# Kernel optimization log

Measured on AMD Instinct MI355X. Metric: run time of the kernel, lower is better.

The kernel has to match this reference:

```python
import jax, jax.numpy as jnp
import numpy as np


def setup_inputs() -> dict:
    key = jax.random.key(0)
    kx, ky = jax.random.split(key)
    x = jax.random.normal(kx, (16, 4096, 3), dtype=jnp.float32)
    y = jax.random.normal(ky, (16, 4096, 3), dtype=jnp.float32)
    return {"x": x, "y": y}


def reference(x, y):
    # avoiding the O(b*N*M*d) difference tensor of the naive expansion.
    x2 = jnp.sum(x * x, axis=-1)                  # (b, N)
    y2 = jnp.sum(y * y, axis=-1)                  # (b, M)
    xy = jnp.einsum('bnd,bmd->bnm', x, y)         # (b, N, M)
    dist = x2[:, :, None] + y2[:, None, :] - 2.0 * xy
    min_d = jnp.min(dist, axis=2)                 # top-1 smallest over M -> (b, N)
    chamfer = jnp.sum(min_d, axis=1) / x.shape[1] # (b,)
    return jnp.sum(chamfer)
```

## Files before the change

### kernel.cpp

```cpp
#include <hip/hip_runtime.h>


constexpr int NPTS   = 4096;
constexpr int NBATCH = 16;
constexpr int BLOCK  = 256;
constexpr int XPT    = 8;
constexpr int XCHUNK = BLOCK * XPT;
constexpr int NXC    = NPTS / XCHUNK;
constexpr int NYC    = 32;
constexpr int YT     = NPTS / NYC;


__global__ __launch_bounds__(BLOCK, 4) void chamfer_part_kernel(
    const float* __restrict__ x, const float* __restrict__ y,
    float* __restrict__ ws, float* __restrict__ out)
{
    __shared__ float4 sy[YT];

    if (blockIdx.x == 0 && threadIdx.x == 0) out[0] = 0.0f;

    const int b      = blockIdx.x / (NXC * NYC);
    const int xchunk = (blockIdx.x / NYC) % NXC;
    const int ychunk = blockIdx.x % NYC;

    for (int i = threadIdx.x; i < YT; i += BLOCK) {
        const float* yp = y + ((size_t)b * NPTS + ychunk * YT + i) * 3;
        const float y0 = yp[0], y1 = yp[1], y2 = yp[2];
        sy[i] = make_float4(2.0f * y0, 2.0f * y1, 2.0f * y2,
                            fmaf(y2, y2, fmaf(y1, y1, y0 * y0)));
    }

    const int xbase = xchunk * XCHUNK + threadIdx.x * XPT;
    const float4* xp4 = (const float4*)(x + ((size_t)b * NPTS + xbase) * 3);
    const float4 a0 = xp4[0], a1 = xp4[1], a2 = xp4[2];
    const float4 a3 = xp4[3], a4 = xp4[4], a5 = xp4[5];
    const float xa[XPT][3] = {
        {a0.x, a0.y, a0.z}, {a0.w, a1.x, a1.y},
        {a1.z, a1.w, a2.x}, {a2.y, a2.z, a2.w},
        {a3.x, a3.y, a3.z}, {a3.w, a4.x, a4.y},
        {a4.z, a4.w, a5.x}, {a5.y, a5.z, a5.w}};

    float x2s[XPT];
    #pragma unroll
    for (int i = 0; i < XPT; ++i)
        x2s[i] = fmaf(xa[i][2], xa[i][2],
                 fmaf(xa[i][1], xa[i][1], xa[i][0] * xa[i][0]));

    __syncthreads();

    float m[XPT];
    #pragma unroll
    for (int i = 0; i < XPT; ++i) m[i] = 3.4e38f;

    #pragma unroll 2
    for (int j = 0; j < YT; j += 4) {
        const float4 Y0 = sy[j + 0];
        const float4 Y1 = sy[j + 1];
        const float4 Y2 = sy[j + 2];
        const float4 Y3 = sy[j + 3];
        #pragma unroll
        for (int i = 0; i < XPT; ++i) {
            const float t0 = fmaf(-xa[i][0], Y0.x,
                             fmaf(-xa[i][1], Y0.y,
                             fmaf(-xa[i][2], Y0.z, Y0.w)));
            const float t1 = fmaf(-xa[i][0], Y1.x,
                             fmaf(-xa[i][1], Y1.y,
                             fmaf(-xa[i][2], Y1.z, Y1.w)));
            const float t2 = fmaf(-xa[i][0], Y2.x,
                             fmaf(-xa[i][1], Y2.y,
                             fmaf(-xa[i][2], Y2.z, Y2.w)));
            const float t3 = fmaf(-xa[i][0], Y3.x,
                             fmaf(-xa[i][1], Y3.y,
                             fmaf(-xa[i][2], Y3.z, Y3.w)));
            m[i] = fminf(fminf(fminf(t0, t1), fminf(t2, t3)), m[i]);
        }
    }

    float* wp = ws + ((size_t)b * NYC + ychunk) * NPTS + xbase;
    #pragma unroll
    for (int i = 0; i < XPT; i += 4) {
        float4 o;
        float* oc = (float*)&o;
        #pragma unroll
        for (int k = 0; k < 4; ++k)
            oc[k] = fmaxf(x2s[i + k] + m[i + k], 0.0f);
        ((float4*)wp)[i / 4] = o;
    }
}


__global__ __launch_bounds__(BLOCK) void chamfer_reduce_kernel(
    const float* __restrict__ ws, float* __restrict__ out)
{
    __shared__ float swsum[BLOCK / 64];
    const int idx = blockIdx.x * BLOCK + threadIdx.x;
    const int b   = idx / NPTS;
    const int xp  = idx % NPTS;

    const float* p = ws + (size_t)b * NYC * NPTS + xp;
    float mn = 3.4e38f;
    #pragma unroll 8
    for (int yc = 0; yc < NYC; ++yc)
        mn = fminf(mn, p[(size_t)yc * NPTS]);

    float s = mn;
    for (int off = 32; off > 0; off >>= 1)
        s += __shfl_down(s, off, 64);
    const int wave = threadIdx.x >> 6;
    if ((threadIdx.x & 63) == 0) swsum[wave] = s;
    __syncthreads();
    if (threadIdx.x == 0) {
        float t = 0.f;
        #pragma unroll
        for (int w = 0; w < BLOCK / 64; ++w) t += swsum[w];
        atomicAdd(out, t * (1.0f / NPTS));
    }
}


__global__ __launch_bounds__(BLOCK) void chamfer_min_atomic_kernel(
    const float* __restrict__ x, const float* __restrict__ y,
    unsigned int* __restrict__ ws_min)
{
    constexpr int YTILE = 256;
    constexpr int FNYC  = NPTS / YTILE;
    __shared__ float4 sy[YTILE];

    const int b      = blockIdx.x / (NXC * FNYC);
    const int xchunk = (blockIdx.x / FNYC) % NXC;
    const int ychunk = blockIdx.x % FNYC;

    {
        const float* yp = y + ((size_t)b * NPTS + ychunk * YTILE + threadIdx.x) * 3;
        const float y0 = yp[0], y1 = yp[1], y2 = yp[2];
        sy[threadIdx.x] = make_float4(2.0f * y0, 2.0f * y1, 2.0f * y2,
                                      fmaf(y2, y2, fmaf(y1, y1, y0 * y0)));
    }

    const int xbase = xchunk * XCHUNK + threadIdx.x * XPT;
    const float4* xp4 = (const float4*)(x + ((size_t)b * NPTS + xbase) * 3);
    const float4 a0 = xp4[0], a1 = xp4[1], a2 = xp4[2];
    const float4 a3 = xp4[3], a4 = xp4[4], a5 = xp4[5];
    const float xa[XPT][3] = {
        {a0.x, a0.y, a0.z}, {a0.w, a1.x, a1.y},
        {a1.z, a1.w, a2.x}, {a2.y, a2.z, a2.w},
        {a3.x, a3.y, a3.z}, {a3.w, a4.x, a4.y},
        {a4.z, a4.w, a5.x}, {a5.y, a5.z, a5.w}};

    float x2s[XPT];
    #pragma unroll
    for (int i = 0; i < XPT; ++i)
        x2s[i] = fmaf(xa[i][2], xa[i][2],
                 fmaf(xa[i][1], xa[i][1], xa[i][0] * xa[i][0]));

    __syncthreads();

    float m[XPT];
    #pragma unroll
    for (int i = 0; i < XPT; ++i) m[i] = 3.4e38f;

    #pragma unroll 2
    for (int j = 0; j < YTILE; j += 2) {
        const float4 Y0 = sy[j];
        const float4 Y1 = sy[j + 1];
        #pragma unroll
        for (int i = 0; i < XPT; ++i) {
            const float t0 = fmaf(-xa[i][0], Y0.x,
                             fmaf(-xa[i][1], Y0.y,
                             fmaf(-xa[i][2], Y0.z, Y0.w)));
            const float t1 = fmaf(-xa[i][0], Y1.x,
                             fmaf(-xa[i][1], Y1.y,
                             fmaf(-xa[i][2], Y1.z, Y1.w)));
            m[i] = fminf(m[i], fminf(t0, t1));
        }
    }

    unsigned int* wm = ws_min + (size_t)b * NPTS + xbase;
    #pragma unroll
    for (int i = 0; i < XPT; ++i) {
        const float d = fmaxf(x2s[i] + m[i], 0.0f);
        atomicMin(&wm[i], __float_as_uint(d));
    }
}

__global__ __launch_bounds__(BLOCK) void chamfer_sum_kernel(
    const unsigned int* __restrict__ ws_min, float* __restrict__ out)
{
    __shared__ float swsum[BLOCK / 64];
    const int total = NBATCH * NPTS;
    float s = 0.f;
    for (int i = blockIdx.x * BLOCK + threadIdx.x; i < total;
         i += gridDim.x * BLOCK)
        s += __uint_as_float(ws_min[i]);

    for (int off = 32; off > 0; off >>= 1)
        s += __shfl_down(s, off, 64);
    const int wave = threadIdx.x >> 6;
    if ((threadIdx.x & 63) == 0) swsum[wave] = s;
    __syncthreads();
    if (threadIdx.x == 0) {
        float t = 0.f;
        #pragma unroll
        for (int w = 0; w < BLOCK / 64; ++w) t += swsum[w];
        atomicAdd(out, t * (1.0f / NPTS));
    }
}


extern "C" void kernel_launch(void* const* d_in, const int* in_sizes, int n_in,
                              void* d_out, int out_size, void* d_ws, size_t ws_size,
                              hipStream_t stream) {
    const float* x = (const float*)d_in[0];
    const float* y = (const float*)d_in[1];
    float* out = (float*)d_out;

    const size_t need = (size_t)NBATCH * NYC * NPTS * sizeof(float);

    if (ws_size >= need) {
        float* ws = (float*)d_ws;
        chamfer_part_kernel<<<NBATCH * NXC * NYC, BLOCK, 0, stream>>>(
            x, y, ws, out);
        chamfer_reduce_kernel<<<NBATCH * NPTS / BLOCK, BLOCK, 0, stream>>>(
            ws, out);
    } else {
        unsigned int* ws_min = (unsigned int*)d_ws;
        hipMemsetAsync(out, 0, sizeof(float), stream);
        hipMemsetAsync(ws_min, 0xFF, (size_t)NBATCH * NPTS * sizeof(unsigned int),
                       stream);
        chamfer_min_atomic_kernel<<<NBATCH * NXC * 16, BLOCK, 0, stream>>>(
            x, y, ws_min);
        chamfer_sum_kernel<<<64, BLOCK, 0, stream>>>(ws_min, out);
    }
}
```

Before: 86.78 us.

## Broadcast y points via readlane into SGPRs instead of LDS staging

Drops the shared-memory staging of the y tile and its block barrier. Each wave now loads 64 y points per iteration straight from global memory into registers and broadcasts each one to the whole wave with readlane, so the inner loop reads y from scalar registers rather than LDS. The x squared norm is computed at the end to free registers. Each wave now loads and preprocesses the y tile separately, so global y traffic is duplicated across the four waves, and readlane adds scalar-pipe work and latency.

```diff
diff --git a/kernel.cpp b/kernel.cpp
--- a/kernel.cpp
+++ b/kernel.cpp
@@ -1,5 +1,9 @@
 #include <hip/hip_runtime.h>
 
+
+__device__ __forceinline__ float rlane(float v, int k) {
+    return __int_as_float(__builtin_amdgcn_readlane(__float_as_int(v), k));
+}
 
 constexpr int NPTS   = 4096;
 constexpr int NBATCH = 16;
@@ -15,20 +19,12 @@
     const float* __restrict__ x, const float* __restrict__ y,
     float* __restrict__ ws, float* __restrict__ out)
 {
-    __shared__ float4 sy[YT];
-
     if (blockIdx.x == 0 && threadIdx.x == 0) out[0] = 0.0f;
 
     const int b      = blockIdx.x / (NXC * NYC);
     const int xchunk = (blockIdx.x / NYC) % NXC;
     const int ychunk = blockIdx.x % NYC;
-
-    for (int i = threadIdx.x; i < YT; i += BLOCK) {
-        const float* yp = y + ((size_t)b * NPTS + ychunk * YT + i) * 3;
-        const float y0 = yp[0], y1 = yp[1], y2 = yp[2];
-        sy[i] = make_float4(2.0f * y0, 2.0f * y1, 2.0f * y2,
-                            fmaf(y2, y2, fmaf(y1, y1, y0 * y0)));
-    }
+    const int lane   = threadIdx.x & 63;
 
     const int xbase = xchunk * XCHUNK + threadIdx.x * XPT;
     const float4* xp4 = (const float4*)(x + ((size_t)b * NPTS + xbase) * 3);
@@ -40,39 +36,37 @@
         {a3.x, a3.y, a3.z}, {a3.w, a4.x, a4.y},
         {a4.z, a4.w, a5.x}, {a5.y, a5.z, a5.w}};
 
-    float x2s[XPT];
-    #pragma unroll
-    for (int i = 0; i < XPT; ++i)
-        x2s[i] = fmaf(xa[i][2], xa[i][2],
-                 fmaf(xa[i][1], xa[i][1], xa[i][0] * xa[i][0]));
-
-    __syncthreads();
-
     float m[XPT];
     #pragma unroll
     for (int i = 0; i < XPT; ++i) m[i] = 3.4e38f;
 
-    #pragma unroll 2
-    for (int j = 0; j < YT; j += 4) {
-        const float4 Y0 = sy[j + 0];
-        const float4 Y1 = sy[j + 1];
-        const float4 Y2 = sy[j + 2];
-        const float4 Y3 = sy[j + 3];
-        #pragma unroll
-        for (int i = 0; i < XPT; ++i) {
-            const float t0 = fmaf(-xa[i][0], Y0.x,
-                             fmaf(-xa[i][1], Y0.y,
-                             fmaf(-xa[i][2], Y0.z, Y0.w)));
-            const float t1 = fmaf(-xa[i][0], Y1.x,
-                             fmaf(-xa[i][1], Y1.y,
-                             fmaf(-xa[i][2], Y1.z, Y1.w)));
-            const float t2 = fmaf(-xa[i][0], Y2.x,
-                             fmaf(-xa[i][1], Y2.y,
-                             fmaf(-xa[i][2], Y2.z, Y2.w)));
-            const float t3 = fmaf(-xa[i][0], Y3.x,
-                             fmaf(-xa[i][1], Y3.y,
-                             fmaf(-xa[i][2], Y3.z, Y3.w)));
-            m[i] = fminf(fminf(fminf(t0, t1), fminf(t2, t3)), m[i]);
+    const float* ybase = y + ((size_t)b * NPTS + ychunk * YT) * 3;
+
+    #pragma unroll 1
+    for (int tt = 0; tt < YT / 64; ++tt) {
+        const float* yp = ybase + (tt * 64 + lane) * 3;
+        const float y0 = yp[0], y1 = yp[1], y2 = yp[2];
+        const float p0 = 2.0f * y0;
+        const float p1 = 2.0f * y1;
+        const float p2 = 2.0f * y2;
+        const float pn = fmaf(y2, y2, fmaf(y1, y1, y0 * y0));
+
+        #pragma unroll
+        for (int k = 0; k < 64; k += 2) {
+            const float q0 = rlane(p0, k),     q1 = rlane(p1, k);
+            const float q2 = rlane(p2, k),     qn = rlane(pn, k);
+            const float r0 = rlane(p0, k + 1), r1 = rlane(p1, k + 1);
+            const float r2 = rlane(p2, k + 1), rn = rlane(pn, k + 1);
+            #pragma unroll
+            for (int i = 0; i < XPT; ++i) {
+                const float t0 = fmaf(-xa[i][0], q0,
+                                 fmaf(-xa[i][1], q1,
+                                 fmaf(-xa[i][2], q2, qn)));
+                const float t1 = fmaf(-xa[i][0], r0,
+                                 fmaf(-xa[i][1], r1,
+                                 fmaf(-xa[i][2], r2, rn)));
+                m[i] = fminf(fminf(t0, t1), m[i]);
+            }
         }
     }
 
@@ -82,8 +76,13 @@
         float4 o;
         float* oc = (float*)&o;
         #pragma unroll
-        for (int k = 0; k < 4; ++k)
-            oc[k] = fmaxf(x2s[i + k] + m[i + k], 0.0f);
+        for (int k = 0; k < 4; ++k) {
+            const int p = i + k;
+            const float x2 = fmaf(xa[p][2], xa[p][2],
+                             fmaf(xa[p][1], xa[p][1],
+                                  xa[p][0] * xa[p][0]));
+            oc[k] = fmaxf(x2 + m[p], 0.0f);
+        }
         ((float4*)wp)[i / 4] = o;
     }
 }
```

Result: slower. 95.31 us (+9.8%).
